# Optimization experiments

Measured on AMD Instinct MI355X. Metric: run time of the kernel, lower is better.

## Reference

```python
import jax, jax.numpy as jnp
import numpy as np

B, L, D, H = 2, 2048, 1024, 16
DK = D // H


def setup_inputs() -> dict:
    key = jax.random.key(0)
    ks = jax.random.split(key, 12)
    s = 1.0 / np.sqrt(D)
    inp = {
        "query": jax.random.normal(ks[0], (B, L, D), jnp.float32),
        "key_": jax.random.normal(ks[1], (B, L, D), jnp.float32),
        "value": jax.random.normal(ks[2], (B, L, D), jnp.float32),
        # causal boolean mask, broadcast over heads: (B, 1, L_q, L_k)
        "mask": jnp.broadcast_to(jnp.tril(jnp.ones((L, L), jnp.bool_)), (B, 1, L, L)),
        "w_q": jax.random.uniform(ks[3], (D, D), jnp.float32, -s, s),
        "b_q": jax.random.uniform(ks[4], (D,), jnp.float32, -s, s),
        "w_k": jax.random.uniform(ks[5], (D, D), jnp.float32, -s, s),
        "b_k": jax.random.uniform(ks[6], (D,), jnp.float32, -s, s),
        "w_v": jax.random.uniform(ks[7], (D, D), jnp.float32, -s, s),
        "b_v": jax.random.uniform(ks[8], (D,), jnp.float32, -s, s),
        "w_o": jax.random.uniform(ks[9], (D, D), jnp.float32, -s, s),
        "b_o": jax.random.uniform(ks[10], (D,), jnp.float32, -s, s),
    }
    return inp


def reference(query, key_, value, mask, w_q, b_q, w_k, b_k, w_v, b_v, w_o, b_o):
    # torch nn.Linear: y = x @ W.T + b, weight shape (out, in)
    Q = query @ w_q.T + b_q
    K = key_ @ w_k.T + b_k
    V = value @ w_v.T + b_v
    # (B, L, H, DK) -> (B, H, L, DK)
    Q = Q.reshape(B, L, H, DK).transpose(0, 2, 1, 3)
    K = K.reshape(B, L, H, DK).transpose(0, 2, 1, 3)
    V = V.reshape(B, L, H, DK).transpose(0, 2, 1, 3)
    scaling = jnp.sqrt(jnp.float32(DK))
    scores = jnp.einsum("bhqd,bhkd->bhqk", Q, K) / scaling  # (B,H,L,L)
    scores = jnp.where(mask, scores, jnp.float32(-1e9))
    attn = jax.nn.softmax(scores, axis=-1)
    out = jnp.einsum("bhqk,bhkd->bhqd", attn, V)  # (B,H,L,DK)
    out = out.transpose(0, 2, 1, 3).reshape(B, L, D)
    return out @ w_o.T + b_o
```

## Files before the change

### kernel.cpp

```cpp
#include <hip/hip_runtime.h>
#include <stdint.h>

#define Bb 2
#define Ll 2048
#define Dd 1024
#define Hh 16
#define DKd 64
#define Mm (Bb*Ll)

typedef __bf16 bf16_t;
typedef __bf16 bf16x8 __attribute__((ext_vector_type(8)));
typedef float f32x4 __attribute__((ext_vector_type(4)));
typedef unsigned u32x2 __attribute__((ext_vector_type(2)));

#define AS1C(p) ((const __attribute__((address_space(1))) void*)(p))
#define AS3(p)  ((__attribute__((address_space(3))) void*)(p))

__device__ __forceinline__ unsigned short bfu(float f){
  return __builtin_bit_cast(unsigned short, (bf16_t)f);
}
__device__ __forceinline__ void wait_vm4(){ asm volatile("s_waitcnt vmcnt(4)" ::: "memory"); }
__device__ __forceinline__ void wait_vm6(){ asm volatile("s_waitcnt vmcnt(6)" ::: "memory"); }
__device__ __forceinline__ void wait_vm0(){ asm volatile("s_waitcnt vmcnt(0)" ::: "memory"); }
__device__ __forceinline__ void bar(){
  __builtin_amdgcn_sched_barrier(0);
  __builtin_amdgcn_s_barrier();
  __builtin_amdgcn_sched_barrier(0);
}

struct CvtArgs { const float* in[4]; ushort4* out[4]; };

__global__ void cvt_multi(CvtArgs a, int n4){
  const int z = blockIdx.y;
  const float* in = a.in[z];
  ushort4* out = a.out[z];
  int i = blockIdx.x*256 + threadIdx.x;
  if (i < n4){
    float4 v = ((const float4*)in)[i];
    ushort4 o; o.x=bfu(v.x); o.y=bfu(v.y); o.z=bfu(v.z); o.w=bfu(v.w);
    out[i] = o;
  }
}

__global__ __launch_bounds__(256) void transpose_v(const bf16_t* __restrict__ Vh,
                                                   bf16_t* __restrict__ VT){
  __shared__ bf16_t Tl[64][72];
  const int bh = blockIdx.y;
  const int l0 = blockIdx.x * 64;
  const int tid = threadIdx.x;
  const bf16_t* src = Vh + (size_t)bh*Ll*DKd;
  bf16_t* dst = VT + (size_t)bh*Ll*DKd;
#pragma unroll
  for (int rd = 0; rd < 2; ++rd){
    int l = rd*32 + (tid>>3), dk0 = (tid&7)*8;
    bf16x8 v = *(const bf16x8*)(src + (size_t)(l0+l)*DKd + dk0);
#pragma unroll
    for (int j = 0; j < 8; ++j) Tl[dk0+j][l] = v[j];
  }
  __syncthreads();
#pragma unroll
  for (int rd = 0; rd < 2; ++rd){
    int dk = rd*32 + (tid>>3), lc = (tid&7)*8;
    *(bf16x8*)(dst + (size_t)dk*Ll + l0 + lc) = *(const bf16x8*)&Tl[dk][lc];
  }
}

#define BM 128
#define BN 64
#define BKs 64

struct GemmArgs {
  const bf16_t* A[3];
  const bf16_t* W[3];
  const float*  bias[3];
  void*         out[3];
  float         scale[3];
};

__device__ __forceinline__ void stage_tile(
    const bf16_t* __restrict__ A, const bf16_t* __restrict__ Bw,
    int m0, int n0, int K, int k0, bf16_t* As, bf16_t* Bs,
    int w, int srow, int scol)
{
#pragma unroll
  for (int i = 0; i < 4; i++) {
    int c = i*4 + w;
    int row = c*8 + srow;
    int sc = scol ^ ((row & 7) << 3);
    __builtin_amdgcn_global_load_lds(AS1C(A + (size_t)(m0+row)*K + k0 + sc),
                                     AS3(As + c*512), 16, 0, 0);
  }
#pragma unroll
  for (int i = 0; i < 2; i++) {
    int c = i*4 + w;
    int row = c*8 + srow;
    int sc = scol ^ ((row & 7) << 3);
    __builtin_amdgcn_global_load_lds(AS1C(Bw + (size_t)(n0+row)*K + k0 + sc),
                                     AS3(Bs + c*512), 16, 0, 0);
  }
}

template<int OUTMODE>
__global__ __launch_bounds__(256) void gemm_bt(GemmArgs ga, int M, int N, int K)
{
  const int z = blockIdx.z;
  const bf16_t* __restrict__ A  = ga.A[z];
  const bf16_t* __restrict__ Bw = ga.W[z];
  const float*  __restrict__ bias = ga.bias[z];
  void* __restrict__ out = ga.out[z];
  const float scale = ga.scale[z];

  __shared__ bf16_t As[2][BM*BKs];
  __shared__ bf16_t Bs[2][BN*BKs];
  const int tid = threadIdx.x;
  const int lane = tid & 63;
  const int w = tid >> 6;
  const int m0 = blockIdx.x * BM;
  const int n0 = blockIdx.y * BN;
  const int wr = (w >> 1) * 64, wc = (w & 1) * 32;
  const int lrow16 = lane & 15;
  const int kgrp = lane >> 4;
  const int srow = lane >> 3;
  const int scol = (lane & 7) * 8;

  f32x4 acc[4][2] = {};

  stage_tile(A, Bw, m0, n0, K, 0, As[0], Bs[0], w, srow, scol);

  const int KT = K / BKs;
  int cur = 0;
  for (int kt = 0; kt < KT; ++kt) {
    if (kt + 1 < KT) {
      stage_tile(A, Bw, m0, n0, K, (kt+1)*BKs, As[cur^1], Bs[cur^1], w, srow, scol);
      wait_vm6();
    } else {
      wait_vm0();
    }
    bar();
#pragma unroll
    for (int ks = 0; ks < 2; ++ks) {
      const int kbyte = ks*64 + kgrp*16;
      bf16x8 af[4], bfr[2];
#pragma unroll
      for (int m = 0; m < 4; m++) {
        int row = wr + m*16 + lrow16;
        af[m] = *(const bf16x8*)((const char*)As[cur] + row*128 + (kbyte ^ ((row & 7) << 4)));
      }
#pragma unroll
      for (int n = 0; n < 2; n++) {
        int row = wc + n*16 + lrow16;
        bfr[n] = *(const bf16x8*)((const char*)Bs[cur] + row*128 + (kbyte ^ ((row & 7) << 4)));
      }
#pragma unroll
      for (int m = 0; m < 4; m++)
#pragma unroll
        for (int n = 0; n < 2; n++)
          acc[m][n] = __builtin_amdgcn_mfma_f32_16x16x32_bf16(af[m], bfr[n], acc[m][n], 0, 0, 0);
    }
    bar();
    cur ^= 1;
  }

#pragma unroll
  for (int m = 0; m < 4; m++)
#pragma unroll
    for (int n = 0; n < 2; n++)
#pragma unroll
      for (int i = 0; i < 4; i++) {
        int row = m0 + wr + m*16 + kgrp*4 + i;
        int col = n0 + wc + n*16 + lrow16;
        float v = (acc[m][n][i] + bias[col]) * scale;
        if (OUTMODE == 1) {
          ((float*)out)[(size_t)row*N + col] = v;
        } else {
          int b = row >> 11, l = row & 2047;
          int h = col >> 6, dk = col & 63;
          ((unsigned short*)out)[((size_t)((b<<4) + h)*Ll + l)*DKd + dk] = bfu(v);
        }
      }
}

#define KVB 64

__global__ __launch_bounds__(256) void attn_kernel(
    const bf16_t* __restrict__ Qh, const bf16_t* __restrict__ Kh,
    const bf16_t* __restrict__ VTg, unsigned short* __restrict__ Oa)
{
  const int id = blockIdx.x;
  const int x = id & 7;
  const int rest = id >> 3;
  const int hq = rest >> 4;
  const int j  = rest & 15;
  const int bh = x + 8*hq;
  const int qtA = j, qtB = 31 - j;

  const int tid = threadIdx.x, lane = tid & 63, w = tid >> 6;
  const int r = lane & 15, g = lane >> 4;

  const bf16_t* Qp  = Qh  + (size_t)bh * Ll * DKd;
  const bf16_t* Kp  = Kh  + (size_t)bh * Ll * DKd;
  const bf16_t* VTp = VTg + (size_t)bh * Ll * DKd;

  __shared__ bf16_t Klds[2][64*64];
  __shared__ bf16_t Vlds[2][64*64];
  __shared__ bf16_t Plds[4][16*64];

  bf16x8 qf[2], qB[2];
#pragma unroll
  for (int ks = 0; ks < 2; ++ks) {
    qf[ks] = *(const bf16x8*)(Qp + (size_t)(qtA*64 + w*16 + r)*DKd + ks*32 + g*8);
    qB[ks] = *(const bf16x8*)(Qp + (size_t)(qtB*64 + w*16 + r)*DKd + ks*32 + g*8);
  }
  int qb = qtA*64 + w*16;

  bf16x8 ones;
#pragma unroll
  for (int jj = 0; jj < 8; ++jj) ones[jj] = (bf16_t)1.0f;

  f32x4 accO[4] = {};
  f32x4 accL = {};
  float mrow = -1e30f;

  const int krow_l = lane >> 3;
  const int kcol_l = ((lane & 7)*16) ^ (krow_l << 4);
  char* Pw = (char*)&Plds[w][0];
  const int rsw = (r & 7) << 4;
  const int b_ = bh >> 4, h_ = bh & 15;

  auto pre_tiles = [&](int kv, int buf){
#pragma unroll
    for (int i = 0; i < 2; ++i) {
      int c = i*4 + w;
      __builtin_amdgcn_global_load_lds(
        AS1C((const char*)Kp + (size_t)(kv*KVB + c*8 + krow_l)*128 + kcol_l),
        AS3((char*)&Klds[buf][0] + c*1024), 16, 0, 0);
      __builtin_amdgcn_global_load_lds(
        AS1C((const char*)VTp + (size_t)(c*8 + krow_l)*4096 + kv*128 + kcol_l),
        AS3((char*)&Vlds[buf][0] + c*1024), 16, 0, 0);
    }
  };

  pre_tiles(0, 0);

  int cur = 0;
  for (int s = 0; s < 33; ++s) {
    if (s < 32) {
      int kv2 = (s < j) ? s + 1 : s - j;
      pre_tiles(kv2, cur^1);
      wait_vm4();
    } else {
      wait_vm0();
    }
    bar();

    const int kv0 = ((s <= j) ? s : s - j - 1) * KVB;

    const char* Kbase = (const char*)&Klds[cur][0];
    f32x4 sv[4] = {};
    __builtin_amdgcn_s_setprio(1);
#pragma unroll
    for (int ks = 0; ks < 2; ++ks) {
      const int kbyte = ks*64 + g*16;
#pragma unroll
      for (int n = 0; n < 4; ++n) {
        int row = n*16 + r;
        bf16x8 kf = *(const bf16x8*)(Kbase + row*128 + (kbyte ^ ((row & 7) << 4)));
        sv[n] = __builtin_amdgcn_mfma_f32_16x16x32_bf16(kf, qf[ks], sv[n], 0, 0, 0);
      }
    }
    __builtin_amdgcn_s_setprio(0);

    if (s == j || s == 32) {
      const int qg = qb + r;
#pragma unroll
      for (int n = 0; n < 4; ++n)
#pragma unroll
        for (int i = 0; i < 4; ++i)
          if (kv0 + n*16 + g*4 + i > qg) sv[n][i] = -1e30f;
    }

    float m0 = fmaxf(fmaxf(sv[0][0], sv[0][1]), sv[0][2]);
    float m1 = fmaxf(fmaxf(sv[0][3], sv[1][0]), sv[1][1]);
    float m2 = fmaxf(fmaxf(sv[1][2], sv[1][3]), sv[2][0]);
    float m3 = fmaxf(fmaxf(sv[2][1], sv[2][2]), sv[2][3]);
    float m4 = fmaxf(fmaxf(sv[3][0], sv[3][1]), sv[3][2]);
    float mx = fmaxf(fmaxf(fmaxf(m0, m1), m2), fmaxf(fmaxf(m3, m4), sv[3][3]));
    if (__any(mx > mrow + 8.f)) {
      mx = fmaxf(mx, __shfl_xor(mx, 16));
      mx = fmaxf(mx, __shfl_xor(mx, 32));
      float mnew = fmaxf(mrow, mx);
      float corr = __builtin_amdgcn_exp2f(mrow - mnew);
      float c0 = __shfl(corr, g*4 + 0);
      float c1 = __shfl(corr, g*4 + 1);
      float c2 = __shfl(corr, g*4 + 2);
      float c3 = __shfl(corr, g*4 + 3);
#pragma unroll
      for (int n = 0; n < 4; ++n) {
        accO[n][0] *= c0; accO[n][1] *= c1; accO[n][2] *= c2; accO[n][3] *= c3;
      }
      accL[0] *= c0; accL[1] *= c1; accL[2] *= c2; accL[3] *= c3;
      mrow = mnew;
    }
#pragma unroll
    for (int n = 0; n < 4; ++n)
#pragma unroll
      for (int i = 0; i < 4; ++i)
        sv[n][i] = __builtin_amdgcn_exp2f(sv[n][i] - mrow);

#pragma unroll
    for (int n = 0; n < 4; ++n) {
      unsigned lo = (unsigned)bfu(sv[n][0]) | ((unsigned)bfu(sv[n][1]) << 16);
      unsigned hi = (unsigned)bfu(sv[n][2]) | ((unsigned)bfu(sv[n][3]) << 16);
      u32x2 pk; pk[0] = lo; pk[1] = hi;
      *(u32x2*)(Pw + r*128 + ((n*32 + g*8) ^ rsw)) = pk;
    }

    const char* Vbase = (const char*)&Vlds[cur][0];
    __builtin_amdgcn_s_setprio(1);
#pragma unroll
    for (int ks = 0; ks < 2; ++ks) {
      const int kbyte = ks*64 + g*16;
      bf16x8 pa = *(const bf16x8*)(Pw + r*128 + (kbyte ^ rsw));
      accL = __builtin_amdgcn_mfma_f32_16x16x32_bf16(pa, ones, accL, 0, 0, 0);
#pragma unroll
      for (int n = 0; n < 4; ++n) {
        int row = n*16 + r;
        bf16x8 vf = *(const bf16x8*)(Vbase + row*128 + (kbyte ^ ((row & 7) << 4)));
        accO[n] = __builtin_amdgcn_mfma_f32_16x16x32_bf16(pa, vf, accO[n], 0, 0, 0);
      }
    }
    __builtin_amdgcn_s_setprio(0);

    if (s == j) {
#pragma unroll
      for (int i = 0; i < 4; ++i) {
        float inv = 1.f / accL[i];
        int q = qb + g*4 + i;
#pragma unroll
        for (int n = 0; n < 4; ++n)
          Oa[((size_t)(b_*Ll + q))*Dd + h_*DKd + n*16 + r] = bfu(accO[n][i] * inv);
      }
#pragma unroll
      for (int n = 0; n < 4; ++n) accO[n] = f32x4{};
      accL = f32x4{};
      mrow = -1e30f;
      qf[0] = qB[0]; qf[1] = qB[1];
      qb = qtB*64 + w*16;
    }

    bar();
    cur ^= 1;
  }

#pragma unroll
  for (int i = 0; i < 4; ++i) {
    float inv = 1.f / accL[i];
    int q = qb + g*4 + i;
#pragma unroll
    for (int n = 0; n < 4; ++n)
      Oa[((size_t)(b_*Ll + q))*Dd + h_*DKd + n*16 + r] = bfu(accO[n][i] * inv);
  }
}

extern "C" void kernel_launch(void* const* d_in, const int* in_sizes, int n_in,
                              void* d_out, int out_size, void* d_ws, size_t ws_size,
                              hipStream_t stream)
{
  const float* q  = (const float*)d_in[0];
  const float* k  = (const float*)d_in[1];
  const float* v  = (const float*)d_in[2];
  const float* wq = (const float*)d_in[4];
  const float* bq = (const float*)d_in[5];
  const float* wk = (const float*)d_in[6];
  const float* bk = (const float*)d_in[7];
  const float* wv = (const float*)d_in[8];
  const float* bv = (const float*)d_in[9];
  const float* wo = (const float*)d_in[10];
  const float* bo = (const float*)d_in[11];

  char* ws = (char*)d_ws;
  bf16_t* Xq = (bf16_t*)(ws + 0);
  bf16_t* Xk = (bf16_t*)(ws + 8388608);
  bf16_t* Xv = (bf16_t*)(ws + 16777216);
  bf16_t* Wq = (bf16_t*)(ws + 25165824);
  bf16_t* Wk = (bf16_t*)(ws + 27262976);
  bf16_t* Wv = (bf16_t*)(ws + 29360128);
  bf16_t* Wo = (bf16_t*)(ws + 31457280);
  bf16_t* Qh = (bf16_t*)(ws + 33554432);
  bf16_t* Kh = (bf16_t*)(ws + 41943040);
  bf16_t* Vh = (bf16_t*)(ws + 50331648);
  bf16_t* Oa = (bf16_t*)(ws + 58720256);
  bf16_t* VT = Xq;

  const int NX = Mm * Dd;
  const int NW = Dd * Dd;

  CvtArgs cx; cx.in[0]=q; cx.in[1]=k; cx.in[2]=v; cx.in[3]=q;
  cx.out[0]=(ushort4*)Xq; cx.out[1]=(ushort4*)Xk; cx.out[2]=(ushort4*)Xv; cx.out[3]=(ushort4*)Xq;
  cvt_multi<<<dim3(NX/4/256, 3), 256, 0, stream>>>(cx, NX/4);

  CvtArgs cw; cw.in[0]=wq; cw.in[1]=wk; cw.in[2]=wv; cw.in[3]=wo;
  cw.out[0]=(ushort4*)Wq; cw.out[1]=(ushort4*)Wk; cw.out[2]=(ushort4*)Wv; cw.out[3]=(ushort4*)Wo;
  cvt_multi<<<dim3(NW/4/256, 4), 256, 0, stream>>>(cw, NW/4);

  const float qscale = 0.125f * 1.4426950408889634f;
  GemmArgs gqkv;
  gqkv.A[0]=Xq; gqkv.A[1]=Xk; gqkv.A[2]=Xv;
  gqkv.W[0]=Wq; gqkv.W[1]=Wk; gqkv.W[2]=Wv;
  gqkv.bias[0]=bq; gqkv.bias[1]=bk; gqkv.bias[2]=bv;
  gqkv.out[0]=Qh; gqkv.out[1]=Kh; gqkv.out[2]=Vh;
  gqkv.scale[0]=qscale; gqkv.scale[1]=1.0f; gqkv.scale[2]=1.0f;
  gemm_bt<0><<<dim3(Mm/BM, Dd/BN, 3), 256, 0, stream>>>(gqkv, Mm, Dd, Dd);

  transpose_v<<<dim3(32, 32), 256, 0, stream>>>(Vh, VT);

  attn_kernel<<<dim3(512), 256, 0, stream>>>(Qh, Kh, VT, (unsigned short*)Oa);

  GemmArgs go;
  go.A[0]=Oa; go.A[1]=Oa; go.A[2]=Oa;
  go.W[0]=Wo; go.W[1]=Wo; go.W[2]=Wo;
  go.bias[0]=bo; go.bias[1]=bo; go.bias[2]=bo;
  go.out[0]=d_out; go.out[1]=d_out; go.out[2]=d_out;
  go.scale[0]=1.0f; go.scale[1]=1.0f; go.scale[2]=1.0f;
  gemm_bt<1><<<dim3(Mm/BM, Dd/BN, 1), 256, 0, stream>>>(go, Mm, Dd, Dd);
}
```

Before: 121.9 us.

## Restructure causal attention to one Q tile per block with two waves

The attention kernel no longer pairs Q tiles (j, 31-j) inside one 256-thread block. It now launches 1024 blocks of 128 threads, each covering a single 64-row Q tile with two waves of 32 rows apiece, and orders blocks heaviest-first for load balance. Each wave computes two 16-row fragments so every K/V fragment read from LDS is reused twice. Separately, the two conversion launches are merged into one seven-slot cvt kernel to save a launch. The trade-off is less work per block and load balance that now depends on the block-ordering heuristic rather than on paired tiles.

```diff
diff --git a/kernel.cpp b/kernel.cpp
--- a/kernel.cpp
+++ b/kernel.cpp
@@ -19,8 +19,8 @@
 __device__ __forceinline__ unsigned short bfu(float f){
   return __builtin_bit_cast(unsigned short, (bf16_t)f);
 }
-__device__ __forceinline__ void wait_vm4(){ asm volatile("s_waitcnt vmcnt(4)" ::: "memory"); }
 __device__ __forceinline__ void wait_vm6(){ asm volatile("s_waitcnt vmcnt(6)" ::: "memory"); }
+__device__ __forceinline__ void wait_vm8(){ asm volatile("s_waitcnt vmcnt(8)" ::: "memory"); }
 __device__ __forceinline__ void wait_vm0(){ asm volatile("s_waitcnt vmcnt(0)" ::: "memory"); }
 __device__ __forceinline__ void bar(){
   __builtin_amdgcn_sched_barrier(0);
@@ -28,17 +28,15 @@
   __builtin_amdgcn_sched_barrier(0);
 }
 
-struct CvtArgs { const float* in[4]; ushort4* out[4]; };
-
-__global__ void cvt_multi(CvtArgs a, int n4){
+struct Cvt7 { const float* in[7]; ushort4* out[7]; int n4[7]; };
+
+__global__ void cvt_multi(Cvt7 a){
   const int z = blockIdx.y;
-  const float* in = a.in[z];
-  ushort4* out = a.out[z];
   int i = blockIdx.x*256 + threadIdx.x;
-  if (i < n4){
-    float4 v = ((const float4*)in)[i];
+  if (i < a.n4[z]){
+    float4 v = ((const float4*)a.in[z])[i];
     ushort4 o; o.x=bfu(v.x); o.y=bfu(v.y); o.z=bfu(v.z); o.w=bfu(v.w);
-    out[i] = o;
+    a.out[z][i] = o;
   }
 }
 
@@ -182,17 +180,25 @@
 
 #define KVB 64
 
-__global__ __launch_bounds__(256) void attn_kernel(
+__global__ __launch_bounds__(128) void attn_kernel(
     const bf16_t* __restrict__ Qh, const bf16_t* __restrict__ Kh,
     const bf16_t* __restrict__ VTg, unsigned short* __restrict__ Oa)
 {
   const int id = blockIdx.x;
-  const int x = id & 7;
-  const int rest = id >> 3;
-  const int hq = rest >> 4;
-  const int j  = rest & 15;
-  const int bh = x + 8*hq;
-  const int qtA = j, qtB = 31 - j;
+  const int xcd = id & 7;
+  const int hq  = (id >> 3) & 3;
+  const int s5  = id >> 5;
+  const int g2 = s5 >> 3, u = s5 & 7;
+  int j;
+  switch (g2) {
+    case 0:  j = 31 - u; break;
+    case 1:  j = u;      break;
+    case 2:  j = 23 - u; break;
+    default: j = 8 + u;  break;
+  }
+  const int bh = xcd + 8*hq;
+  const int q0 = j * 64;
+  const int nkv = j + 1;
 
   const int tid = threadIdx.x, lane = tid & 63, w = tid >> 6;
   const int r = lane & 15, g = lane >> 4;
@@ -203,34 +209,34 @@
 
   __shared__ bf16_t Klds[2][64*64];
   __shared__ bf16_t Vlds[2][64*64];
-  __shared__ bf16_t Plds[4][16*64];
-
-  bf16x8 qf[2], qB[2];
-#pragma unroll
-  for (int ks = 0; ks < 2; ++ks) {
-    qf[ks] = *(const bf16x8*)(Qp + (size_t)(qtA*64 + w*16 + r)*DKd + ks*32 + g*8);
-    qB[ks] = *(const bf16x8*)(Qp + (size_t)(qtB*64 + w*16 + r)*DKd + ks*32 + g*8);
-  }
-  int qb = qtA*64 + w*16;
+  __shared__ bf16_t Plds[2][2][16*64];
+
+  bf16x8 qf[2][2];
+#pragma unroll
+  for (int f = 0; f < 2; ++f)
+#pragma unroll
+    for (int ks = 0; ks < 2; ++ks)
+      qf[f][ks] = *(const bf16x8*)(Qp + (size_t)(q0 + w*32 + f*16 + r)*DKd + ks*32 + g*8);
 
   bf16x8 ones;
 #pragma unroll
   for (int jj = 0; jj < 8; ++jj) ones[jj] = (bf16_t)1.0f;
 
-  f32x4 accO[4] = {};
-  f32x4 accL = {};
-  float mrow = -1e30f;
+  f32x4 accO[2][4] = {};
+  f32x4 accL[2] = {};
+  float mrow[2] = {-1e30f, -1e30f};
 
   const int krow_l = lane >> 3;
   const int kcol_l = ((lane & 7)*16) ^ (krow_l << 4);
-  char* Pw = (char*)&Plds[w][0];
+  char* Pw0 = (char*)&Plds[w][0][0];
+  char* Pw1 = (char*)&Plds[w][1][0];
   const int rsw = (r & 7) << 4;
   const int b_ = bh >> 4, h_ = bh & 15;
 
   auto pre_tiles = [&](int kv, int buf){
 #pragma unroll
-    for (int i = 0; i < 2; ++i) {
-      int c = i*4 + w;
+    for (int i = 0; i < 4; ++i) {
+      int c = i*2 + w;
       __builtin_amdgcn_global_load_lds(
         AS1C((const char*)Kp + (size_t)(kv*KVB + c*8 + krow_l)*128 + kcol_l),
         AS3((char*)&Klds[buf][0] + c*1024), 16, 0, 0);
@@ -243,20 +249,17 @@
   pre_tiles(0, 0);
 
   int cur = 0;
-  for (int s = 0; s < 33; ++s) {
-    if (s < 32) {
-      int kv2 = (s < j) ? s + 1 : s - j;
-      pre_tiles(kv2, cur^1);
-      wait_vm4();
+  for (int s = 0; s < nkv; ++s) {
+    if (s + 1 < nkv) {
+      pre_tiles(s + 1, cur^1);
+      wait_vm8();
     } else {
       wait_vm0();
     }
     bar();
 
-    const int kv0 = ((s <= j) ? s : s - j - 1) * KVB;
-
     const char* Kbase = (const char*)&Klds[cur][0];
-    f32x4 sv[4] = {};
+    f32x4 sv[2][4] = {};
     __builtin_amdgcn_s_setprio(1);
 #pragma unroll
     for (int ks = 0; ks < 2; ++ks) {
@@ -265,54 +268,64 @@
       for (int n = 0; n < 4; ++n) {
         int row = n*16 + r;
         bf16x8 kf = *(const bf16x8*)(Kbase + row*128 + (kbyte ^ ((row & 7) << 4)));
-        sv[n] = __builtin_amdgcn_mfma_f32_16x16x32_bf16(kf, qf[ks], sv[n], 0, 0, 0);
+        sv[0][n] = __builtin_amdgcn_mfma_f32_16x16x32_bf16(kf, qf[0][ks], sv[0][n], 0, 0, 0);
+        sv[1][n] = __builtin_amdgcn_mfma_f32_16x16x32_bf16(kf, qf[1][ks], sv[1][n], 0, 0, 0);
       }
     }
     __builtin_amdgcn_s_setprio(0);
 
-    if (s == j || s == 32) {
-      const int qg = qb + r;
+    if (s == nkv - 1) {
+      const int kv0 = s * KVB;
+#pragma unroll
+      for (int f = 0; f < 2; ++f) {
+        const int qg = q0 + w*32 + f*16 + r;
+#pragma unroll
+        for (int n = 0; n < 4; ++n)
+#pragma unroll
+          for (int i = 0; i < 4; ++i)
+            if (kv0 + n*16 + g*4 + i > qg) sv[f][n][i] = -1e30f;
+      }
+    }
+
+#pragma unroll
+    for (int f = 0; f < 2; ++f) {
+      float m0 = fmaxf(fmaxf(sv[f][0][0], sv[f][0][1]), sv[f][0][2]);
+      float m1 = fmaxf(fmaxf(sv[f][0][3], sv[f][1][0]), sv[f][1][1]);
+      float m2 = fmaxf(fmaxf(sv[f][1][2], sv[f][1][3]), sv[f][2][0]);
+      float m3 = fmaxf(fmaxf(sv[f][2][1], sv[f][2][2]), sv[f][2][3]);
+      float m4 = fmaxf(fmaxf(sv[f][3][0], sv[f][3][1]), sv[f][3][2]);
+      float mx = fmaxf(fmaxf(fmaxf(m0, m1), m2), fmaxf(fmaxf(m3, m4), sv[f][3][3]));
+      if (__any(mx > mrow[f] + 8.f)) {
+        mx = fmaxf(mx, __shfl_xor(mx, 16));
+        mx = fmaxf(mx, __shfl_xor(mx, 32));
+        float mnew = fmaxf(mrow[f], mx);
+        float corr = __builtin_amdgcn_exp2f(mrow[f] - mnew);
+        float c0 = __shfl(corr, g*4 + 0);
+        float c1 = __shfl(corr, g*4 + 1);
+        float c2 = __shfl(corr, g*4 + 2);
+        float c3 = __shfl(corr, g*4 + 3);
+#pragma unroll
+        for (int n = 0; n < 4; ++n) {
+          accO[f][n][0] *= c0; accO[f][n][1] *= c1;
+          accO[f][n][2] *= c2; accO[f][n][3] *= c3;
+        }
+        accL[f][0] *= c0; accL[f][1] *= c1; accL[f][2] *= c2; accL[f][3] *= c3;
+        mrow[f] = mnew;
+      }
 #pragma unroll
       for (int n = 0; n < 4; ++n)
 #pragma unroll
         for (int i = 0; i < 4; ++i)
-          if (kv0 + n*16 + g*4 + i > qg) sv[n][i] = -1e30f;
-    }
-
-    float m0 = fmaxf(fmaxf(sv[0][0], sv[0][1]), sv[0][2]);
-    float m1 = fmaxf(fmaxf(sv[0][3], sv[1][0]), sv[1][1]);
-    float m2 = fmaxf(fmaxf(sv[1][2], sv[1][3]), sv[2][0]);
-    float m3 = fmaxf(fmaxf(sv[2][1], sv[2][2]), sv[2][3]);
-    float m4 = fmaxf(fmaxf(sv[3][0], sv[3][1]), sv[3][2]);
-    float mx = fmaxf(fmaxf(fmaxf(m0, m1), m2), fmaxf(fmaxf(m3, m4), sv[3][3]));
-    if (__any(mx > mrow + 8.f)) {
-      mx = fmaxf(mx, __shfl_xor(mx, 16));
-      mx = fmaxf(mx, __shfl_xor(mx, 32));
-      float mnew = fmaxf(mrow, mx);
-      float corr = __builtin_amdgcn_exp2f(mrow - mnew);
-      float c0 = __shfl(corr, g*4 + 0);
-      float c1 = __shfl(corr, g*4 + 1);
-      float c2 = __shfl(corr, g*4 + 2);
-      float c3 = __shfl(corr, g*4 + 3);
+          sv[f][n][i] = __builtin_amdgcn_exp2f(sv[f][n][i] - mrow[f]);
+
+      char* Pw = f ? Pw1 : Pw0;
 #pragma unroll
       for (int n = 0; n < 4; ++n) {
-        accO[n][0] *= c0; accO[n][1] *= c1; accO[n][2] *= c2; accO[n][3] *= c3;
-      }
-      accL[0] *= c0; accL[1] *= c1; accL[2] *= c2; accL[3] *= c3;
-      mrow = mnew;
-    }
-#pragma unroll
-    for (int n = 0; n < 4; ++n)
-#pragma unroll
-      for (int i = 0; i < 4; ++i)
-        sv[n][i] = __builtin_amdgcn_exp2f(sv[n][i] - mrow);
-
-#pragma unroll
-    for (int n = 0; n < 4; ++n) {
-      unsigned lo = (unsigned)bfu(sv[n][0]) | ((unsigned)bfu(sv[n][1]) << 16);
-      unsigned hi = (unsigned)bfu(sv[n][2]) | ((unsigned)bfu(sv[n][3]) << 16);
-      u32x2 pk; pk[0] = lo; pk[1] = hi;
-      *(u32x2*)(Pw + r*128 + ((n*32 + g*8) ^ rsw)) = pk;
+        unsigned lo = (unsigned)bfu(sv[f][n][0]) | ((unsigned)bfu(sv[f][n][1]) << 16);
+        unsigned hi = (unsigned)bfu(sv[f][n][2]) | ((unsigned)bfu(sv[f][n][3]) << 16);
+        u32x2 pk; pk[0] = lo; pk[1] = hi;
+        *(u32x2*)(Pw + r*128 + ((n*32 + g*8) ^ rsw)) = pk;
+      }
     }
 
     const char* Vbase = (const char*)&Vlds[cur][0];
@@ -320,46 +333,34 @@
 #pragma unroll
     for (int ks = 0; ks < 2; ++ks) {
       const int kbyte = ks*64 + g*16;
-      bf16x8 pa = *(const bf16x8*)(Pw + r*128 + (kbyte ^ rsw));
-      accL = __builtin_amdgcn_mfma_f32_16x16x32_bf16(pa, ones, accL, 0, 0, 0);
+      bf16x8 pa0 = *(const bf16x8*)(Pw0 + r*128 + (kbyte ^ rsw));
+      bf16x8 pa1 = *(const bf16x8*)(Pw1 + r*128 + (kbyte ^ rsw));
+      accL[0] = __builtin_amdgcn_mfma_f32_16x16x32_bf16(pa0, ones, accL[0], 0, 0, 0);
+      accL[1] = __builtin_amdgcn_mfma_f32_16x16x32_bf16(pa1, ones, accL[1], 0, 0, 0);
 #pragma unroll
       for (int n = 0; n < 4; ++n) {
         int row = n*16 + r;
         bf16x8 vf = *(const bf16x8*)(Vbase + row*128 + (kbyte ^ ((row & 7) << 4)));
-        accO[n] = __builtin_amdgcn_mfma_f32_16x16x32_bf16(pa, vf, accO[n], 0, 0, 0);
+        accO[0][n] = __builtin_amdgcn_mfma_f32_16x16x32_bf16(pa0, vf, accO[0][n], 0, 0, 0);
+        accO[1][n] = __builtin_amdgcn_mfma_f32_16x16x32_bf16(pa1, vf, accO[1][n], 0, 0, 0);
       }
     }
     __builtin_amdgcn_s_setprio(0);
-
-    if (s == j) {
-#pragma unroll
-      for (int i = 0; i < 4; ++i) {
-        float inv = 1.f / accL[i];
-        int q = qb + g*4 + i;
-#pragma unroll
-        for (int n = 0; n < 4; ++n)
-          Oa[((size_t)(b_*Ll + q))*Dd + h_*DKd + n*16 + r] = bfu(accO[n][i] * inv);
-      }
-#pragma unroll
-      for (int n = 0; n < 4; ++n) accO[n] = f32x4{};
-      accL = f32x4{};
-      mrow = -1e30f;
-      qf[0] = qB[0]; qf[1] = qB[1];
-      qb = qtB*64 + w*16;
-    }
 
     bar();
     cur ^= 1;
   }
 
 #pragma unroll
-  for (int i = 0; i < 4; ++i) {
-    float inv = 1.f / accL[i];
-    int q = qb + g*4 + i;
-#pragma unroll
-    for (int n = 0; n < 4; ++n)
-      Oa[((size_t)(b_*Ll + q))*Dd + h_*DKd + n*16 + r] = bfu(accO[n][i] * inv);
-  }
+  for (int f = 0; f < 2; ++f)
+#pragma unroll
+    for (int i = 0; i < 4; ++i) {
+      float inv = 1.f / accL[f][i];
+      int q = q0 + w*32 + f*16 + g*4 + i;
+#pragma unroll
+      for (int n = 0; n < 4; ++n)
+        Oa[((size_t)(b_*Ll + q))*Dd + h_*DKd + n*16 + r] = bfu(accO[f][n][i] * inv);
+    }
 }
 
 extern "C" void kernel_launch(void* const* d_in, const int* in_sizes, int n_in,
@@ -392,16 +393,18 @@
   bf16_t* Oa = (bf16_t*)(ws + 58720256);
   bf16_t* VT = Xq;
 
-  const int NX = Mm * Dd;
-  const int NW = Dd * Dd;
-
-  CvtArgs cx; cx.in[0]=q; cx.in[1]=k; cx.in[2]=v; cx.in[3]=q;
-  cx.out[0]=(ushort4*)Xq; cx.out[1]=(ushort4*)Xk; cx.out[2]=(ushort4*)Xv; cx.out[3]=(ushort4*)Xq;
-  cvt_multi<<<dim3(NX/4/256, 3), 256, 0, stream>>>(cx, NX/4);
-
-  CvtArgs cw; cw.in[0]=wq; cw.in[1]=wk; cw.in[2]=wv; cw.in[3]=wo;
-  cw.out[0]=(ushort4*)Wq; cw.out[1]=(ushort4*)Wk; cw.out[2]=(ushort4*)Wv; cw.out[3]=(ushort4*)Wo;
-  cvt_multi<<<dim3(NW/4/256, 4), 256, 0, stream>>>(cw, NW/4);
+  const int NX4 = Mm * Dd / 4;
+  const int NW4 = Dd * Dd / 4;
+
+  Cvt7 cv;
+  cv.in[0]=q;  cv.out[0]=(ushort4*)Xq; cv.n4[0]=NX4;
+  cv.in[1]=k;  cv.out[1]=(ushort4*)Xk; cv.n4[1]=NX4;
+  cv.in[2]=v;  cv.out[2]=(ushort4*)Xv; cv.n4[2]=NX4;
+  cv.in[3]=wq; cv.out[3]=(ushort4*)Wq; cv.n4[3]=NW4;
+  cv.in[4]=wk; cv.out[4]=(ushort4*)Wk; cv.n4[4]=NW4;
+  cv.in[5]=wv; cv.out[5]=(ushort4*)Wv; cv.n4[5]=NW4;
+  cv.in[6]=wo; cv.out[6]=(ushort4*)Wo; cv.n4[6]=NW4;
+  cvt_multi<<<dim3(NX4/256, 7), 256, 0, stream>>>(cv);
 
   const float qscale = 0.125f * 1.4426950408889634f;
   GemmArgs gqkv;
@@ -414,7 +417,7 @@
 
   transpose_v<<<dim3(32, 32), 256, 0, stream>>>(Vh, VT);
 
-  attn_kernel<<<dim3(512), 256, 0, stream>>>(Qh, Kh, VT, (unsigned short*)Oa);
+  attn_kernel<<<dim3(1024), 128, 0, stream>>>(Qh, Kh, VT, (unsigned short*)Oa);
 
   GemmArgs go;
   go.A[0]=Oa; go.A[1]=Oa; go.A[2]=Oa;
```

New measurement: 129.7 us. 6.4% more time.

## Fuse V transpose into QKV GEMM epilogue and load V fragments from global

Applied to the files above, without the earlier changes.

The QKV projection epilogue now writes V directly in transposed (bh, dk, l) layout with vectorized ushort4 stores, which removes the separate transpose kernel. The two conversion launches are merged into one seven-way launch. In attention, V is no longer staged through LDS: each wave loads its V MFMA fragments straight from global into registers at the top of each iteration, and the vmcnt waits are adjusted for this. The attention grid ordering is also remapped. The cost is a runtime mode branch in the GEMM epilogue, more register pressure, and V global latency that is exposed rather than double-buffered.

```diff
diff --git a/kernel.cpp b/kernel.cpp
--- a/kernel.cpp
+++ b/kernel.cpp
@@ -19,49 +19,25 @@
 __device__ __forceinline__ unsigned short bfu(float f){
   return __builtin_bit_cast(unsigned short, (bf16_t)f);
 }
-__device__ __forceinline__ void wait_vm4(){ asm volatile("s_waitcnt vmcnt(4)" ::: "memory"); }
-__device__ __forceinline__ void wait_vm6(){ asm volatile("s_waitcnt vmcnt(6)" ::: "memory"); }
-__device__ __forceinline__ void wait_vm0(){ asm volatile("s_waitcnt vmcnt(0)" ::: "memory"); }
+__device__ __forceinline__ void wait_vm6(){  asm volatile("s_waitcnt vmcnt(6)"  ::: "memory"); }
+__device__ __forceinline__ void wait_vm8(){  asm volatile("s_waitcnt vmcnt(8)"  ::: "memory"); }
+__device__ __forceinline__ void wait_vm10(){ asm volatile("s_waitcnt vmcnt(10)" ::: "memory"); }
+__device__ __forceinline__ void wait_vm0(){  asm volatile("s_waitcnt vmcnt(0)"  ::: "memory"); }
 __device__ __forceinline__ void bar(){
   __builtin_amdgcn_sched_barrier(0);
   __builtin_amdgcn_s_barrier();
   __builtin_amdgcn_sched_barrier(0);
 }
 
-struct CvtArgs { const float* in[4]; ushort4* out[4]; };
-
-__global__ void cvt_multi(CvtArgs a, int n4){
+struct Cvt7 { const float* in[7]; ushort4* out[7]; int n4[7]; };
+
+__global__ void cvt_multi(Cvt7 a){
   const int z = blockIdx.y;
-  const float* in = a.in[z];
-  ushort4* out = a.out[z];
   int i = blockIdx.x*256 + threadIdx.x;
-  if (i < n4){
-    float4 v = ((const float4*)in)[i];
+  if (i < a.n4[z]){
+    float4 v = ((const float4*)a.in[z])[i];
     ushort4 o; o.x=bfu(v.x); o.y=bfu(v.y); o.z=bfu(v.z); o.w=bfu(v.w);
-    out[i] = o;
-  }
-}
-
-__global__ __launch_bounds__(256) void transpose_v(const bf16_t* __restrict__ Vh,
-                                                   bf16_t* __restrict__ VT){
-  __shared__ bf16_t Tl[64][72];
-  const int bh = blockIdx.y;
-  const int l0 = blockIdx.x * 64;
-  const int tid = threadIdx.x;
-  const bf16_t* src = Vh + (size_t)bh*Ll*DKd;
-  bf16_t* dst = VT + (size_t)bh*Ll*DKd;
-#pragma unroll
-  for (int rd = 0; rd < 2; ++rd){
-    int l = rd*32 + (tid>>3), dk0 = (tid&7)*8;
-    bf16x8 v = *(const bf16x8*)(src + (size_t)(l0+l)*DKd + dk0);
-#pragma unroll
-    for (int j = 0; j < 8; ++j) Tl[dk0+j][l] = v[j];
-  }
-  __syncthreads();
-#pragma unroll
-  for (int rd = 0; rd < 2; ++rd){
-    int dk = rd*32 + (tid>>3), lc = (tid&7)*8;
-    *(bf16x8*)(dst + (size_t)dk*Ll + l0 + lc) = *(const bf16x8*)&Tl[dk][lc];
+    a.out[z][i] = o;
   }
 }
 
@@ -75,6 +51,7 @@
   const float*  bias[3];
   void*         out[3];
   float         scale[3];
+  int           mode[3];
 };
 
 __device__ __forceinline__ void stage_tile(
@@ -100,7 +77,6 @@
   }
 }
 
-template<int OUTMODE>
 __global__ __launch_bounds__(256) void gemm_bt(GemmArgs ga, int M, int N, int K)
 {
   const int z = blockIdx.z;
@@ -109,6 +85,7 @@
   const float*  __restrict__ bias = ga.bias[z];
   void* __restrict__ out = ga.out[z];
   const float scale = ga.scale[z];
+  const int mode = ga.mode[z];
 
   __shared__ bf16_t As[2][BM*BKs];
   __shared__ bf16_t Bs[2][BN*BKs];
@@ -164,20 +141,34 @@
 #pragma unroll
   for (int m = 0; m < 4; m++)
 #pragma unroll
-    for (int n = 0; n < 2; n++)
-#pragma unroll
-      for (int i = 0; i < 4; i++) {
-        int row = m0 + wr + m*16 + kgrp*4 + i;
-        int col = n0 + wc + n*16 + lrow16;
-        float v = (acc[m][n][i] + bias[col]) * scale;
-        if (OUTMODE == 1) {
-          ((float*)out)[(size_t)row*N + col] = v;
-        } else {
-          int b = row >> 11, l = row & 2047;
-          int h = col >> 6, dk = col & 63;
-          ((unsigned short*)out)[((size_t)((b<<4) + h)*Ll + l)*DKd + dk] = bfu(v);
+    for (int n = 0; n < 2; n++) {
+      const int row0 = m0 + wr + m*16 + kgrp*4;
+      const int col  = n0 + wc + n*16 + lrow16;
+      const float bcol = bias[col];
+      if (mode == 2) {
+        int b = row0 >> 11, l0 = row0 & 2047;
+        int h = col >> 6, dk = col & 63;
+        ushort4 u;
+        u.x = bfu((acc[m][n][0] + bcol) * scale);
+        u.y = bfu((acc[m][n][1] + bcol) * scale);
+        u.z = bfu((acc[m][n][2] + bcol) * scale);
+        u.w = bfu((acc[m][n][3] + bcol) * scale);
+        *(ushort4*)((unsigned short*)out + ((size_t)((b<<4) + h)*DKd + dk)*Ll + l0) = u;
+      } else {
+#pragma unroll
+        for (int i = 0; i < 4; i++) {
+          int row = row0 + i;
+          float v = (acc[m][n][i] + bcol) * scale;
+          if (mode == 1) {
+            ((float*)out)[(size_t)row*N + col] = v;
+          } else {
+            int b = row >> 11, l = row & 2047;
+            int h = col >> 6, dk = col & 63;
+            ((unsigned short*)out)[((size_t)((b<<4) + h)*Ll + l)*DKd + dk] = bfu(v);
+          }
         }
       }
+    }
 }
 
 #define KVB 64
@@ -187,12 +178,12 @@
     const bf16_t* __restrict__ VTg, unsigned short* __restrict__ Oa)
 {
   const int id = blockIdx.x;
-  const int x = id & 7;
-  const int rest = id >> 3;
-  const int hq = rest >> 4;
-  const int j  = rest & 15;
-  const int bh = x + 8*hq;
-  const int qtA = j, qtB = 31 - j;
+  const int xcd = id & 7;
+  const int hq  = (id >> 3) & 3;
+  const int j   = id >> 5;
+  const int bh  = xcd + 8*hq;
+  const int sA  = j;
+  const int qtB = 31 - j;
 
   const int tid = threadIdx.x, lane = tid & 63, w = tid >> 6;
   const int r = lane & 15, g = lane >> 4;
@@ -202,16 +193,15 @@
   const bf16_t* VTp = VTg + (size_t)bh * Ll * DKd;
 
   __shared__ bf16_t Klds[2][64*64];
-  __shared__ bf16_t Vlds[2][64*64];
   __shared__ bf16_t Plds[4][16*64];
 
+  int q0 = j * 64;
   bf16x8 qf[2], qB[2];
 #pragma unroll
   for (int ks = 0; ks < 2; ++ks) {
-    qf[ks] = *(const bf16x8*)(Qp + (size_t)(qtA*64 + w*16 + r)*DKd + ks*32 + g*8);
+    qf[ks] = *(const bf16x8*)(Qp + (size_t)(q0 + w*16 + r)*DKd + ks*32 + g*8);
     qB[ks] = *(const bf16x8*)(Qp + (size_t)(qtB*64 + w*16 + r)*DKd + ks*32 + g*8);
   }
-  int qb = qtA*64 + w*16;
 
   bf16x8 ones;
 #pragma unroll
@@ -227,33 +217,37 @@
   const int rsw = (r & 7) << 4;
   const int b_ = bh >> 4, h_ = bh & 15;
 
-  auto pre_tiles = [&](int kv, int buf){
+  auto pre_K = [&](int kv, int buf){
 #pragma unroll
     for (int i = 0; i < 2; ++i) {
       int c = i*4 + w;
       __builtin_amdgcn_global_load_lds(
         AS1C((const char*)Kp + (size_t)(kv*KVB + c*8 + krow_l)*128 + kcol_l),
         AS3((char*)&Klds[buf][0] + c*1024), 16, 0, 0);
-      __builtin_amdgcn_global_load_lds(
-        AS1C((const char*)VTp + (size_t)(c*8 + krow_l)*4096 + kv*128 + kcol_l),
-        AS3((char*)&Vlds[buf][0] + c*1024), 16, 0, 0);
     }
   };
 
-  pre_tiles(0, 0);
+  pre_K(0, 0);
 
   int cur = 0;
   for (int s = 0; s < 33; ++s) {
+    const int kv0 = ((s <= sA) ? s : s - sA - 1) * KVB;
+
+    bf16x8 vfg[2][4];
+#pragma unroll
+    for (int ks = 0; ks < 2; ++ks)
+#pragma unroll
+      for (int n = 0; n < 4; ++n)
+        vfg[ks][n] = *(const bf16x8*)(VTp + (size_t)(n*16 + r)*Ll + kv0 + ks*32 + g*8);
+
     if (s < 32) {
-      int kv2 = (s < j) ? s + 1 : s - j;
-      pre_tiles(kv2, cur^1);
-      wait_vm4();
+      int kv2 = (s < sA) ? s + 1 : s - sA;
+      pre_K(kv2, cur^1);
+      wait_vm10();
     } else {
-      wait_vm0();
+      wait_vm8();
     }
     bar();
-
-    const int kv0 = ((s <= j) ? s : s - j - 1) * KVB;
 
     const char* Kbase = (const char*)&Klds[cur][0];
     f32x4 sv[4] = {};
@@ -270,8 +264,8 @@
     }
     __builtin_amdgcn_s_setprio(0);
 
-    if (s == j || s == 32) {
-      const int qg = qb + r;
+    if (s == sA || s == 32) {
+      const int qg = q0 + w*16 + r;
 #pragma unroll
       for (int n = 0; n < 4; ++n)
 #pragma unroll
@@ -315,7 +309,6 @@
       *(u32x2*)(Pw + r*128 + ((n*32 + g*8) ^ rsw)) = pk;
     }
 
-    const char* Vbase = (const char*)&Vlds[cur][0];
     __builtin_amdgcn_s_setprio(1);
 #pragma unroll
     for (int ks = 0; ks < 2; ++ks) {
@@ -323,29 +316,26 @@
       bf16x8 pa = *(const bf16x8*)(Pw + r*128 + (kbyte ^ rsw));
       accL = __builtin_amdgcn_mfma_f32_16x16x32_bf16(pa, ones, accL, 0, 0, 0);
 #pragma unroll
-      for (int n = 0; n < 4; ++n) {
-        int row = n*16 + r;
-        bf16x8 vf = *(const bf16x8*)(Vbase + row*128 + (kbyte ^ ((row & 7) << 4)));
-        accO[n] = __builtin_amdgcn_mfma_f32_16x16x32_bf16(pa, vf, accO[n], 0, 0, 0);
-      }
+      for (int n = 0; n < 4; ++n)
+        accO[n] = __builtin_amdgcn_mfma_f32_16x16x32_bf16(pa, vfg[ks][n], accO[n], 0, 0, 0);
     }
     __builtin_amdgcn_s_setprio(0);
 
-    if (s == j) {
+    if (s == sA) {
 #pragma unroll
       for (int i = 0; i < 4; ++i) {
         float inv = 1.f / accL[i];
-        int q = qb + g*4 + i;
+        int q = q0 + w*16 + g*4 + i;
 #pragma unroll
         for (int n = 0; n < 4; ++n)
           Oa[((size_t)(b_*Ll + q))*Dd + h_*DKd + n*16 + r] = bfu(accO[n][i] * inv);
       }
+      q0 = qtB * 64;
+      qf[0] = qB[0]; qf[1] = qB[1];
 #pragma unroll
       for (int n = 0; n < 4; ++n) accO[n] = f32x4{};
       accL = f32x4{};
       mrow = -1e30f;
-      qf[0] = qB[0]; qf[1] = qB[1];
-      qb = qtB*64 + w*16;
     }
 
     bar();
@@ -355,7 +345,7 @@
 #pragma unroll
   for (int i = 0; i < 4; ++i) {
     float inv = 1.f / accL[i];
-    int q = qb + g*4 + i;
+    int q = q0 + w*16 + g*4 + i;
 #pragma unroll
     for (int n = 0; n < 4; ++n)
       Oa[((size_t)(b_*Ll + q))*Dd + h_*DKd + n*16 + r] = bfu(accO[n][i] * inv);
@@ -388,31 +378,31 @@
   bf16_t* Wo = (bf16_t*)(ws + 31457280);
   bf16_t* Qh = (bf16_t*)(ws + 33554432);
   bf16_t* Kh = (bf16_t*)(ws + 41943040);
-  bf16_t* Vh = (bf16_t*)(ws + 50331648);
+  bf16_t* VT = (bf16_t*)(ws + 50331648);
   bf16_t* Oa = (bf16_t*)(ws + 58720256);
-  bf16_t* VT = Xq;
-
-  const int NX = Mm * Dd;
-  const int NW = Dd * Dd;
-
-  CvtArgs cx; cx.in[0]=q; cx.in[1]=k; cx.in[2]=v; cx.in[3]=q;
-  cx.out[0]=(ushort4*)Xq; cx.out[1]=(ushort4*)Xk; cx.out[2]=(ushort4*)Xv; cx.out[3]=(ushort4*)Xq;
-  cvt_multi<<<dim3(NX/4/256, 3), 256, 0, stream>>>(cx, NX/4);
-
-  CvtArgs cw; cw.in[0]=wq; cw.in[1]=wk; cw.in[2]=wv; cw.in[3]=wo;
-  cw.out[0]=(ushort4*)Wq; cw.out[1]=(ushort4*)Wk; cw.out[2]=(ushort4*)Wv; cw.out[3]=(ushort4*)Wo;
-  cvt_multi<<<dim3(NW/4/256, 4), 256, 0, stream>>>(cw, NW/4);
+
+  const int NX4 = Mm * Dd / 4;
+  const int NW4 = Dd * Dd / 4;
+
+  Cvt7 cv;
+  cv.in[0]=q;  cv.out[0]=(ushort4*)Xq; cv.n4[0]=NX4;
+  cv.in[1]=k;  cv.out[1]=(ushort4*)Xk; cv.n4[1]=NX4;
+  cv.in[2]=v;  cv.out[2]=(ushort4*)Xv; cv.n4[2]=NX4;
+  cv.in[3]=wq; cv.out[3]=(ushort4*)Wq; cv.n4[3]=NW4;
+  cv.in[4]=wk; cv.out[4]=(ushort4*)Wk; cv.n4[4]=NW4;
+  cv.in[5]=wv; cv.out[5]=(ushort4*)Wv; cv.n4[5]=NW4;
+  cv.in[6]=wo; cv.out[6]=(ushort4*)Wo; cv.n4[6]=NW4;
+  cvt_multi<<<dim3(NX4/256, 7), 256, 0, stream>>>(cv);
 
   const float qscale = 0.125f * 1.4426950408889634f;
   GemmArgs gqkv;
   gqkv.A[0]=Xq; gqkv.A[1]=Xk; gqkv.A[2]=Xv;
   gqkv.W[0]=Wq; gqkv.W[1]=Wk; gqkv.W[2]=Wv;
   gqkv.bias[0]=bq; gqkv.bias[1]=bk; gqkv.bias[2]=bv;
-  gqkv.out[0]=Qh; gqkv.out[1]=Kh; gqkv.out[2]=Vh;
+  gqkv.out[0]=Qh; gqkv.out[1]=Kh; gqkv.out[2]=VT;
   gqkv.scale[0]=qscale; gqkv.scale[1]=1.0f; gqkv.scale[2]=1.0f;
-  gemm_bt<0><<<dim3(Mm/BM, Dd/BN, 3), 256, 0, stream>>>(gqkv, Mm, Dd, Dd);
-
-  transpose_v<<<dim3(32, 32), 256, 0, stream>>>(Vh, VT);
+  gqkv.mode[0]=0; gqkv.mode[1]=0; gqkv.mode[2]=2;
+  gemm_bt<<<dim3(Mm/BM, Dd/BN, 3), 256, 0, stream>>>(gqkv, Mm, Dd, Dd);
 
   attn_kernel<<<dim3(512), 256, 0, stream>>>(Qh, Kh, VT, (unsigned short*)Oa);
 
@@ -422,5 +412,6 @@
   go.bias[0]=bo; go.bias[1]=bo; go.bias[2]=bo;
   go.out[0]=d_out; go.out[1]=d_out; go.out[2]=d_out;
   go.scale[0]=1.0f; go.scale[1]=1.0f; go.scale[2]=1.0f;
-  gemm_bt<1><<<dim3(Mm/BM, Dd/BN, 1), 256, 0, stream>>>(go, Mm, Dd, Dd);
-}
+  go.mode[0]=1; go.mode[1]=1; go.mode[2]=1;
+  gemm_bt<<<dim3(Mm/BM, Dd/BN, 1), 256, 0, stream>>>(go, Mm, Dd, Dd);
+}
```

After: 142.3 us. 1.17x slower.
